# Kernel tuning notes

Measured on AMD Instinct MI355X. Metric: run time of the kernel, lower is better.

The kernel has to match this reference:

```python
import jax, jax.numpy as jnp
import numpy as np

DIM = 512
DIM_INPUTS = (8,)*4 + (16,)*4 + (32,)*4 + (64,)*4 + (128,)*4 + (256,)*4  # 24 bands, sum=2016
N_BANDS = len(DIM_INPUTS)
TOTAL_OUT2 = 2 * sum(DIM_INPUTS)  # 4032 (concatenated last-layer gated width)
B, T = 4, 512


def _glu_tanh(z):
    # LinearGLUWithTanH epilogue: chunk last dim, tanh(a) * sigmoid(gate)
    a, gate = jnp.split(z, 2, axis=-1)
    return jnp.tanh(a) * jax.nn.sigmoid(gate)


def setup_inputs() -> dict:
    key = jax.random.key(0)
    k0, k1, k2, k3, k4 = jax.random.split(key, 5)
    x = jax.random.normal(k0, (B, T, N_BANDS, DIM), dtype=jnp.float32)
    # layer 0: per-band Linear(DIM, 2*DIM), stacked over bands
    W0 = jax.random.normal(k1, (N_BANDS, DIM, 2 * DIM), dtype=jnp.float32) / np.float32(np.sqrt(DIM))
    b0 = jax.random.normal(k2, (N_BANDS, 2 * DIM), dtype=jnp.float32) * 0.01
    # layer 1 (last): per-band Linear(DIM, 2*dim_in); widths differ, so pack
    # all bands' weight columns into one concatenated matrix sliced statically.
    W1 = jax.random.normal(k3, (DIM, TOTAL_OUT2), dtype=jnp.float32) / np.float32(np.sqrt(DIM))
    b1 = jax.random.normal(k4, (TOTAL_OUT2,), dtype=jnp.float32) * 0.01
    return {"x": x, "W0": W0, "b0": b0, "W1": W1, "b1": b1}


def reference(x, W0, b0, W1, b1):
    # layer 0 for all bands in one grouped GEMM: (b t n d),(n d e)->(b t n e)
    h = _glu_tanh(jnp.einsum('btnd,nde->btne', x, W0) + b0)  # (B,T,N,DIM)
    outs = []
    off = 0
    for i, di in enumerate(DIM_INPUTS):  # static loop over structurally distinct bands
        w = W1[:, off:off + 2 * di]
        bb = b1[off:off + 2 * di]
        outs.append(_glu_tanh(h[:, :, i] @ w + bb))  # (B,T,di)
        off += 2 * di
    return jnp.concatenate(outs, axis=-1)  # (B,T,sum(DIM_INPUTS))
```

## Files before the change

kernel.cpp:

```cpp
#include <hip/hip_runtime.h>
#include <cstdint>
#include <cstddef>


typedef _Float16 f16;
typedef _Float16 f16x8 __attribute__((ext_vector_type(8)));
typedef float floatx4 __attribute__((ext_vector_type(4)));

#define BT 2048
#define NB 24

__device__ __forceinline__ int band_di(int b){ return 8 << (b >> 2); }
__device__ __forceinline__ int band_off2(int b){
  int g = b >> 2;
  return 2 * (32 * ((1 << g) - 1) + (b & 3) * (8 << g));
}

__device__ __forceinline__ float fsigm(float x){
  return __builtin_amdgcn_rcpf(1.f + __expf(-x));
}
__device__ __forceinline__ float ftanh(float x){
  return 1.f - 2.f * __builtin_amdgcn_rcpf(1.f + __expf(2.f * x));
}

__device__ __forceinline__ void gl_lds16(const void* g, void* l){
  __builtin_amdgcn_global_load_lds(
      (const __attribute__((address_space(1))) unsigned int*)g,
      (__attribute__((address_space(3))) unsigned int*)l, 16, 0, 0);
}


__global__ __launch_bounds__(256) void cast_x(const float4* __restrict__ in,
                                              f16* __restrict__ out){
  int t = blockIdx.x * 256 + threadIdx.x;
  float4 v = in[t];
  typedef _Float16 f16x4 __attribute__((ext_vector_type(4)));
  f16x4 o = { (f16)v.x, (f16)v.y, (f16)v.z, (f16)v.w };
  *(f16x4*)(out + (size_t)t * 4) = o;
}

__global__ __launch_bounds__(256) void cast_w0(const float* __restrict__ W0,
                                               f16* __restrict__ w0t){
  __shared__ float tile[64][33];
  int bid = blockIdx.x;
  int dt   = bid & 7;
  int half = (bid >> 3) & 1;
  int g    = (bid >> 4) & 15;
  int band = bid >> 8;
  int t = threadIdx.x;
  int c0 = half * 512 + g * 32;
  int d0 = dt * 64;
  int r  = t >> 2;
  int cs = (t & 3) * 8;
  const float* src = W0 + ((size_t)(band * 512 + d0 + r)) * 1024 + c0 + cs;
  float4 v0 = *(const float4*)src;
  float4 v1 = *(const float4*)(src + 4);
  tile[r][cs + 0] = v0.x; tile[r][cs + 1] = v0.y; tile[r][cs + 2] = v0.z; tile[r][cs + 3] = v0.w;
  tile[r][cs + 4] = v1.x; tile[r][cs + 5] = v1.y; tile[r][cs + 6] = v1.z; tile[r][cs + 7] = v1.w;
  __syncthreads();
  int i   = t >> 3;
  int ds8 = (t & 7) * 8;
  int prow = g * 64 + 2 * i + half;
  f16x8 o;
  #pragma unroll
  for (int k = 0; k < 8; ++k) o[k] = (f16)tile[ds8 + k][i];
  *(f16x8*)(w0t + ((size_t)(band * 1024 + prow)) * 512 + d0 + ds8) = o;
}

__global__ __launch_bounds__(256) void cast_w1(const float* __restrict__ W1,
                                               f16* __restrict__ w1t){
  __shared__ f16 tile[16][520];
  int jt = blockIdx.x;
  int j16 = jt * 16;
  int band = 23;
  for (int b = 0; b < 24; ++b){ if (j16 < band_off2(b + 1)) { band = b; break; } }
  int off2 = band_off2(band), di = band_di(band);
  int p0 = j16 - off2;
  int oca = off2 + (p0 >> 1);
  int ocg = oca + di;
  int t = threadIdx.x;
  #pragma unroll
  for (int hh = 0; hh < 2; ++hh){
    int d = hh * 256 + t;
    const float* rowp = W1 + (size_t)d * 4032;
    float4 a0 = *(const float4*)(rowp + oca);
    float4 a1 = *(const float4*)(rowp + oca + 4);
    float4 g0 = *(const float4*)(rowp + ocg);
    float4 g1 = *(const float4*)(rowp + ocg + 4);
    float av[8] = {a0.x,a0.y,a0.z,a0.w,a1.x,a1.y,a1.z,a1.w};
    float gv[8] = {g0.x,g0.y,g0.z,g0.w,g1.x,g1.y,g1.z,g1.w};
    #pragma unroll
    for (int q = 0; q < 8; ++q){
      tile[2*q][d]   = (f16)av[q];
      tile[2*q+1][d] = (f16)gv[q];
    }
  }
  __syncthreads();
  int j = t & 15, dc = (t >> 4) * 32;
  f16x8 o[4];
  #pragma unroll
  for (int k = 0; k < 4; ++k) o[k] = *(const f16x8*)&tile[j][dc + k*8];
  f16* dst = w1t + (size_t)(j16 + j) * 512 + dc;
  #pragma unroll
  for (int k = 0; k < 4; ++k) *(f16x8*)(dst + k*8) = o[k];
}

__global__ __launch_bounds__(256) void cast_bias(const float* __restrict__ b0,
                                                 const float* __restrict__ b1,
                                                 float* __restrict__ b0p,
                                                 float* __restrict__ b1p){
  int t = blockIdx.x * 256 + threadIdx.x;
  if (t < NB * 1024){
    int p = t & 1023;
    int base = t & ~1023;
    b0p[t] = b0[base + ((p & 1) ? 512 + (p >> 1) : (p >> 1))];
  } else {
    int j = t - NB * 1024;
    if (j < 4032){
      int band = 23;
      for (int b = 0; b < 24; ++b){ if (j < band_off2(b + 1)) { band = b; break; } }
      int off2 = band_off2(band);
      int di = band_di(band);
      int p = j - off2;
      b1p[j] = b1[off2 + ((p & 1) ? di + (p >> 1) : (p >> 1))];
    }
  }
}

__global__ __launch_bounds__(256) void gemm1(const f16* __restrict__ xh,
                                             const f16* __restrict__ w0t,
                                             const float* __restrict__ b0p,
                                             f16* __restrict__ h){
  __shared__ __align__(16) f16 As[128 * 64];
  __shared__ __align__(16) f16 Bs[128 * 64];
  int bid = blockIdx.x;
  int wid = (bid & 7) * 384 + (bid >> 3);
  int band = wid >> 7;
  int mt = (wid >> 3) & 15;
  int nt = wid & 7;
  int t = threadIdx.x;
  int lane = t & 63, w = t >> 6;
  int wm = w & 1, wn = w >> 1;
  int quad = lane >> 4, lc = lane & 15;
  const int mrow0 = mt * 128;
  const int nrow0 = nt * 128;

  const char* gA[4]; const char* gB[4];
  f16* lA[4]; f16* lB[4];
  #pragma unroll
  for (int p = 0; p < 4; ++p){
    int idx = p * 256 + t;
    int r = idx >> 3, s = idx & 7, l = s ^ (r & 7);
    gA[p] = (const char*)(xh + ((size_t)(mrow0 + r) * 24 + band) * 512 + l * 8);
    gB[p] = (const char*)(w0t + ((size_t)(band * 1024 + nrow0 + r)) * 512 + l * 8);
    lA[p] = &As[idx * 8];
    lB[p] = &Bs[idx * 8];
  }
  int aoff[4], boff[4];
  #pragma unroll
  for (int i = 0; i < 4; ++i){
    int m = wm * 64 + i * 16 + lc;
    aoff[i] = (m * 64 + ((quad ^ (m & 7)) << 3)) * 2;
    int n = wn * 64 + i * 16 + lc;
    boff[i] = (n * 64 + ((quad ^ (n & 7)) << 3)) * 2;
  }
  const char* Ab = (const char*)As;
  const char* Bb = (const char*)Bs;

  floatx4 acc[4][4];
  #pragma unroll
  for (int i = 0; i < 4; ++i)
    #pragma unroll
    for (int j = 0; j < 4; ++j) acc[i][j] = floatx4{0.f, 0.f, 0.f, 0.f};

  for (int kb = 0; kb < 8; ++kb){
    #pragma unroll
    for (int p = 0; p < 4; ++p){ gl_lds16(gA[p], lA[p]); gA[p] += 128; }
    #pragma unroll
    for (int p = 0; p < 4; ++p){ gl_lds16(gB[p], lB[p]); gB[p] += 128; }
    __syncthreads();
    #pragma unroll
    for (int s2 = 0; s2 < 2; ++s2){
      f16x8 af[4], bf[4];
      #pragma unroll
      for (int i = 0; i < 4; ++i){
        af[i] = *(const f16x8*)(Ab + (aoff[i] ^ (s2 * 64)));
        bf[i] = *(const f16x8*)(Bb + (boff[i] ^ (s2 * 64)));
      }
      #pragma unroll
      for (int i = 0; i < 4; ++i)
        #pragma unroll
        for (int j = 0; j < 4; ++j)
          acc[i][j] = __builtin_amdgcn_mfma_f32_16x16x32_f16(af[i], bf[j], acc[i][j], 0, 0, 0);
    }
    __syncthreads();
  }
  #pragma unroll
  for (int j = 0; j < 4; ++j){
    int colp = nrow0 + wn * 64 + j * 16 + lc;
    float bias = b0p[band * 1024 + colp];
    #pragma unroll
    for (int i = 0; i < 4; ++i){
      int mbase = mrow0 + wm * 64 + i * 16 + quad * 4;
      #pragma unroll
      for (int r = 0; r < 4; ++r){
        float z = acc[i][j][r] + bias;
        float zp = __shfl_xor(z, 1);
        if (!(lc & 1)){
          float hv = ftanh(z) * fsigm(zp);
          h[((size_t)band * BT + mbase + r) * 512 + (colp >> 1)] = (f16)hv;
        }
      }
    }
  }
}

template<int BN>
__device__ __forceinline__ void gemm2_tile(const f16* __restrict__ hb,
                                           const f16* __restrict__ w1t,
                                           const float* __restrict__ b1p,
                                           float* __restrict__ out,
                                           int band, int mt, int ntile,
                                           f16* As, f16* Bs){
  constexpr int WNW = (BN == 128) ? 2 : 1;
  constexpr int WMW = 4 / WNW;
  constexpr int MF = 128 / (WMW * 16);
  constexpr int NF = BN / (WNW * 16);
  int t = threadIdx.x;
  int lane = t & 63, w = t >> 6;
  int wm = (WNW == 2) ? (w & 1) : w;
  int wn = (WNW == 2) ? (w >> 1) : 0;
  int quad = lane >> 4, lc = lane & 15;
  int off2 = band_off2(band);
  int jbase = off2 + ntile * BN;

  constexpr int BCH = BN * 8;
  constexpr int BP = (BCH + 255) / 256;
  const char* gA[4]; const char* gB[BP];
  f16* lA[4]; f16* lB[BP];
  #pragma unroll
  for (int p = 0; p < 4; ++p){
    int idx = p * 256 + t;
    int r = idx >> 3, s = idx & 7, l = s ^ (r & 7);
    gA[p] = (const char*)(hb + ((size_t)(mt * 128 + r)) * 512 + l * 8);
    lA[p] = &As[idx * 8];
  }
  #pragma unroll
  for (int p = 0; p < BP; ++p){
    int idx = p * 256 + t;
    int r = idx >> 3, s = idx & 7, l = s ^ (r & 7);
    gB[p] = (const char*)(w1t + ((size_t)(jbase + r)) * 512 + l * 8);
    lB[p] = &Bs[idx * 8];
  }
  int aoff[MF], boff[NF];
  #pragma unroll
  for (int i = 0; i < MF; ++i){
    int m = wm * (MF * 16) + i * 16 + lc;
    aoff[i] = (m * 64 + ((quad ^ (m & 7)) << 3)) * 2;
  }
  #pragma unroll
  for (int j = 0; j < NF; ++j){
    int n = wn * (NF * 16) + j * 16 + lc;
    boff[j] = (n * 64 + ((quad ^ (n & 7)) << 3)) * 2;
  }
  const char* Ab = (const char*)As;
  const char* Bb = (const char*)Bs;

  floatx4 acc[MF][NF];
  #pragma unroll
  for (int i = 0; i < MF; ++i)
    #pragma unroll
    for (int j = 0; j < NF; ++j) acc[i][j] = floatx4{0.f, 0.f, 0.f, 0.f};

  for (int kb = 0; kb < 8; ++kb){
    #pragma unroll
    for (int p = 0; p < 4; ++p){ gl_lds16(gA[p], lA[p]); gA[p] += 128; }
    #pragma unroll
    for (int p = 0; p < BP; ++p){
      if ((BCH % 256 == 0) || (p * 256 + t) < BCH){
        gl_lds16(gB[p], lB[p]); gB[p] += 128;
      }
    }
    __syncthreads();
    #pragma unroll
    for (int s2 = 0; s2 < 2; ++s2){
      f16x8 af[MF], bf[NF];
      #pragma unroll
      for (int i = 0; i < MF; ++i)
        af[i] = *(const f16x8*)(Ab + (aoff[i] ^ (s2 * 64)));
      #pragma unroll
      for (int j = 0; j < NF; ++j)
        bf[j] = *(const f16x8*)(Bb + (boff[j] ^ (s2 * 64)));
      #pragma unroll
      for (int i = 0; i < MF; ++i)
        #pragma unroll
        for (int j = 0; j < NF; ++j)
          acc[i][j] = __builtin_amdgcn_mfma_f32_16x16x32_f16(af[i], bf[j], acc[i][j], 0, 0, 0);
    }
    __syncthreads();
  }
  int outbase = off2 >> 1;
  #pragma unroll
  for (int j = 0; j < NF; ++j){
    int p = ntile * BN + wn * (NF * 16) + j * 16 + lc;
    float bias = b1p[off2 + p];
    #pragma unroll
    for (int i = 0; i < MF; ++i){
      int mbase = mt * 128 + wm * (MF * 16) + i * 16 + quad * 4;
      #pragma unroll
      for (int r = 0; r < 4; ++r){
        float z = acc[i][j][r] + bias;
        float zp = __shfl_xor(z, 1);
        if (!(lc & 1)){
          out[(size_t)(mbase + r) * 2016 + outbase + (p >> 1)] = ftanh(z) * fsigm(zp);
        }
      }
    }
  }
}

__global__ __launch_bounds__(256) void gemm2(const f16* __restrict__ h,
                                             const f16* __restrict__ w1t,
                                             const float* __restrict__ b1p,
                                             float* __restrict__ out){
  __shared__ __align__(16) f16 As[128 * 64];
  __shared__ __align__(16) f16 Bs[128 * 64];
  int bid = blockIdx.x;
  int band, mt, ntile, cls;
  if (bid < 256){
    band = bid >> 4; mt = bid & 15; ntile = 0; cls = band >> 2;
  } else if (bid < 384){
    int rel = bid - 256; band = 16 + (rel >> 5);
    int r2 = rel & 31; mt = r2 & 15; ntile = r2 >> 4; cls = 4;
  } else {
    int rel = bid - 384; band = 20 + (rel >> 6);
    int r2 = rel & 63; mt = r2 & 15; ntile = r2 >> 4; cls = 5;
  }
  const f16* hb = h + ((size_t)band << 20);
  switch (cls){
    case 0:  gemm2_tile<16 >(hb, w1t, b1p, out, band, mt, ntile, As, Bs); break;
    case 1:  gemm2_tile<32 >(hb, w1t, b1p, out, band, mt, ntile, As, Bs); break;
    case 2:  gemm2_tile<64 >(hb, w1t, b1p, out, band, mt, ntile, As, Bs); break;
    default: gemm2_tile<128>(hb, w1t, b1p, out, band, mt, ntile, As, Bs); break;
  }
}

extern "C" void kernel_launch(void* const* d_in, const int* in_sizes, int n_in,
                              void* d_out, int out_size, void* d_ws, size_t ws_size,
                              hipStream_t stream){
  const float* x  = (const float*)d_in[0];
  const float* W0 = (const float*)d_in[1];
  const float* b0 = (const float*)d_in[2];
  const float* W1 = (const float*)d_in[3];
  const float* b1 = (const float*)d_in[4];
  char* ws = (char*)d_ws;
  f16*   xh   = (f16*)(ws);
  f16*   hbuf = (f16*)(ws + 50331648);
  f16*   w0t  = (f16*)(ws + 100663296);
  f16*   w1t  = (f16*)(ws + 125829120);
  float* b0p  = (float*)(ws + 129957888);
  float* b1p  = (float*)(ws + 130056192);

  cast_x   <<<24576, 256, 0, stream>>>((const float4*)x, xh);
  cast_w0  <<<6144,  256, 0, stream>>>(W0, w0t);
  cast_w1  <<<252,   256, 0, stream>>>(W1, w1t);
  cast_bias<<<112,   256, 0, stream>>>(b0, b1, b0p, b1p);
  gemm1    <<<3072,  256, 0, stream>>>(xh, w0t, b0p, hbuf);
  gemm2    <<<640,   256, 0, stream>>>(hbuf, w1t, b1p, (float*)d_out);
}
```

Baseline: 317.6 us.

## Fuse prep casts into one kernel and load GEMM fragments directly from global

Merges the four cast kernels into a single prep launch and reorders x to a band-major f16 layout during the cast. Both GEMMs drop the LDS staging through global_load_lds and instead have each lane read its MFMA fragments straight from global memory, relying on cache hits and removing the barriers. The GLU epilogue now evaluates tanh or sigmoid once per lane before the shuffle, so no lane computes both. Without LDS, operand reuse across waves depends on L1/L2 hits, and the per-lane 16-byte strided reads may be less efficient than the staged tiles.

```diff
diff --git a/kernel.cpp b/kernel.cpp
--- a/kernel.cpp
+++ b/kernel.cpp
@@ -23,116 +23,117 @@
   return 1.f - 2.f * __builtin_amdgcn_rcpf(1.f + __expf(2.f * x));
 }
 
-__device__ __forceinline__ void gl_lds16(const void* g, void* l){
-  __builtin_amdgcn_global_load_lds(
-      (const __attribute__((address_space(1))) unsigned int*)g,
-      (__attribute__((address_space(3))) unsigned int*)l, 16, 0, 0);
-}
-
-
-__global__ __launch_bounds__(256) void cast_x(const float4* __restrict__ in,
-                                              f16* __restrict__ out){
-  int t = blockIdx.x * 256 + threadIdx.x;
-  float4 v = in[t];
-  typedef _Float16 f16x4 __attribute__((ext_vector_type(4)));
-  f16x4 o = { (f16)v.x, (f16)v.y, (f16)v.z, (f16)v.w };
-  *(f16x4*)(out + (size_t)t * 4) = o;
-}
-
-__global__ __launch_bounds__(256) void cast_w0(const float* __restrict__ W0,
-                                               f16* __restrict__ w0t){
-  __shared__ float tile[64][33];
+__global__ __launch_bounds__(256) void prep(const float* __restrict__ x,
+                                            const float* __restrict__ W0,
+                                            const float* __restrict__ W1,
+                                            const float* __restrict__ b0,
+                                            const float* __restrict__ b1,
+                                            f16* __restrict__ xh2,
+                                            f16* __restrict__ w0t,
+                                            f16* __restrict__ w1t,
+                                            float* __restrict__ b0p,
+                                            float* __restrict__ b1p){
+  __shared__ __align__(16) char smem[33792];
   int bid = blockIdx.x;
-  int dt   = bid & 7;
-  int half = (bid >> 3) & 1;
-  int g    = (bid >> 4) & 15;
-  int band = bid >> 8;
   int t = threadIdx.x;
-  int c0 = half * 512 + g * 32;
-  int d0 = dt * 64;
-  int r  = t >> 2;
-  int cs = (t & 3) * 8;
-  const float* src = W0 + ((size_t)(band * 512 + d0 + r)) * 1024 + c0 + cs;
-  float4 v0 = *(const float4*)src;
-  float4 v1 = *(const float4*)(src + 4);
-  tile[r][cs + 0] = v0.x; tile[r][cs + 1] = v0.y; tile[r][cs + 2] = v0.z; tile[r][cs + 3] = v0.w;
-  tile[r][cs + 4] = v1.x; tile[r][cs + 5] = v1.y; tile[r][cs + 6] = v1.z; tile[r][cs + 7] = v1.w;
-  __syncthreads();
-  int i   = t >> 3;
-  int ds8 = (t & 7) * 8;
-  int prow = g * 64 + 2 * i + half;
-  f16x8 o;
-  #pragma unroll
-  for (int k = 0; k < 8; ++k) o[k] = (f16)tile[ds8 + k][i];
-  *(f16x8*)(w0t + ((size_t)(band * 1024 + prow)) * 512 + d0 + ds8) = o;
-}
-
-__global__ __launch_bounds__(256) void cast_w1(const float* __restrict__ W1,
-                                               f16* __restrict__ w1t){
-  __shared__ f16 tile[16][520];
-  int jt = blockIdx.x;
-  int j16 = jt * 16;
-  int band = 23;
-  for (int b = 0; b < 24; ++b){ if (j16 < band_off2(b + 1)) { band = b; break; } }
-  int off2 = band_off2(band), di = band_di(band);
-  int p0 = j16 - off2;
-  int oca = off2 + (p0 >> 1);
-  int ocg = oca + di;
-  int t = threadIdx.x;
-  #pragma unroll
-  for (int hh = 0; hh < 2; ++hh){
-    int d = hh * 256 + t;
-    const float* rowp = W1 + (size_t)d * 4032;
-    float4 a0 = *(const float4*)(rowp + oca);
-    float4 a1 = *(const float4*)(rowp + oca + 4);
-    float4 g0 = *(const float4*)(rowp + ocg);
-    float4 g1 = *(const float4*)(rowp + ocg + 4);
-    float av[8] = {a0.x,a0.y,a0.z,a0.w,a1.x,a1.y,a1.z,a1.w};
-    float gv[8] = {g0.x,g0.y,g0.z,g0.w,g1.x,g1.y,g1.z,g1.w};
-    #pragma unroll
-    for (int q = 0; q < 8; ++q){
-      tile[2*q][d]   = (f16)av[q];
-      tile[2*q+1][d] = (f16)gv[q];
-    }
-  }
-  __syncthreads();
-  int j = t & 15, dc = (t >> 4) * 32;
-  f16x8 o[4];
-  #pragma unroll
-  for (int k = 0; k < 4; ++k) o[k] = *(const f16x8*)&tile[j][dc + k*8];
-  f16* dst = w1t + (size_t)(j16 + j) * 512 + dc;
-  #pragma unroll
-  for (int k = 0; k < 4; ++k) *(f16x8*)(dst + k*8) = o[k];
-}
-
-__global__ __launch_bounds__(256) void cast_bias(const float* __restrict__ b0,
-                                                 const float* __restrict__ b1,
-                                                 float* __restrict__ b0p,
-                                                 float* __restrict__ b1p){
-  int t = blockIdx.x * 256 + threadIdx.x;
-  if (t < NB * 1024){
-    int p = t & 1023;
-    int base = t & ~1023;
-    b0p[t] = b0[base + ((p & 1) ? 512 + (p >> 1) : (p >> 1))];
+  if (bid < 6144){
+    int r = bid / 3, bg = bid - 3 * r;
+    int band = bg * 8 + (t >> 5);
+    int k16 = (t & 31) * 16;
+    const float* src = x + ((size_t)(r * 24 + band)) * 512 + k16;
+    float4 v0 = *(const float4*)(src + 0);
+    float4 v1 = *(const float4*)(src + 4);
+    float4 v2 = *(const float4*)(src + 8);
+    float4 v3 = *(const float4*)(src + 12);
+    f16x8 o0 = { (f16)v0.x,(f16)v0.y,(f16)v0.z,(f16)v0.w,
+                 (f16)v1.x,(f16)v1.y,(f16)v1.z,(f16)v1.w };
+    f16x8 o1 = { (f16)v2.x,(f16)v2.y,(f16)v2.z,(f16)v2.w,
+                 (f16)v3.x,(f16)v3.y,(f16)v3.z,(f16)v3.w };
+    f16* dst = xh2 + ((size_t)(band * 2048 + r)) * 512 + k16;
+    *(f16x8*)(dst + 0) = o0;
+    *(f16x8*)(dst + 8) = o1;
+  } else if (bid < 12288){
+    float (*tile)[33] = (float(*)[33])smem;
+    int b2 = bid - 6144;
+    int dt   = b2 & 7;
+    int half = (b2 >> 3) & 1;
+    int g    = (b2 >> 4) & 15;
+    int band = b2 >> 8;
+    int c0 = half * 512 + g * 32;
+    int d0 = dt * 64;
+    int r  = t >> 2;
+    int cs = (t & 3) * 8;
+    const float* src = W0 + ((size_t)(band * 512 + d0 + r)) * 1024 + c0 + cs;
+    float4 v0 = *(const float4*)src;
+    float4 v1 = *(const float4*)(src + 4);
+    tile[r][cs+0]=v0.x; tile[r][cs+1]=v0.y; tile[r][cs+2]=v0.z; tile[r][cs+3]=v0.w;
+    tile[r][cs+4]=v1.x; tile[r][cs+5]=v1.y; tile[r][cs+6]=v1.z; tile[r][cs+7]=v1.w;
+    __syncthreads();
+    int i   = t >> 3;
+    int ds8 = (t & 7) * 8;
+    int prow = g * 64 + 2 * i + half;
+    f16x8 o;
+    #pragma unroll
+    for (int k = 0; k < 8; ++k) o[k] = (f16)tile[ds8 + k][i];
+    *(f16x8*)(w0t + ((size_t)(band * 1024 + prow)) * 512 + d0 + ds8) = o;
+  } else if (bid < 12540){
+    f16 (*tw)[520] = (f16(*)[520])smem;
+    int jt = bid - 12288;
+    int j16 = jt * 16;
+    int band = 23;
+    for (int b = 0; b < 24; ++b){ if (j16 < band_off2(b + 1)) { band = b; break; } }
+    int off2 = band_off2(band), di = band_di(band);
+    int p0 = j16 - off2;
+    int oca = off2 + (p0 >> 1);
+    int ocg = oca + di;
+    #pragma unroll
+    for (int hh = 0; hh < 2; ++hh){
+      int d = hh * 256 + t;
+      const float* rowp = W1 + (size_t)d * 4032;
+      float4 a0 = *(const float4*)(rowp + oca);
+      float4 a1 = *(const float4*)(rowp + oca + 4);
+      float4 g0 = *(const float4*)(rowp + ocg);
+      float4 g1 = *(const float4*)(rowp + ocg + 4);
+      float av[8] = {a0.x,a0.y,a0.z,a0.w,a1.x,a1.y,a1.z,a1.w};
+      float gv[8] = {g0.x,g0.y,g0.z,g0.w,g1.x,g1.y,g1.z,g1.w};
+      #pragma unroll
+      for (int q = 0; q < 8; ++q){
+        tw[2*q][d]   = (f16)av[q];
+        tw[2*q+1][d] = (f16)gv[q];
+      }
+    }
+    __syncthreads();
+    int j = t & 15, dc = (t >> 4) * 32;
+    f16x8 o[4];
+    #pragma unroll
+    for (int k = 0; k < 4; ++k) o[k] = *(const f16x8*)&tw[j][dc + k*8];
+    f16* dst = w1t + (size_t)(j16 + j) * 512 + dc;
+    #pragma unroll
+    for (int k = 0; k < 4; ++k) *(f16x8*)(dst + k*8) = o[k];
   } else {
-    int j = t - NB * 1024;
-    if (j < 4032){
-      int band = 23;
-      for (int b = 0; b < 24; ++b){ if (j < band_off2(b + 1)) { band = b; break; } }
-      int off2 = band_off2(band);
-      int di = band_di(band);
-      int p = j - off2;
-      b1p[j] = b1[off2 + ((p & 1) ? di + (p >> 1) : (p >> 1))];
-    }
-  }
-}
-
-__global__ __launch_bounds__(256) void gemm1(const f16* __restrict__ xh,
+    int idx = (bid - 12540) * 256 + t;
+    if (idx < NB * 1024){
+      int p = idx & 1023;
+      int base = idx & ~1023;
+      b0p[idx] = b0[base + ((p & 1) ? 512 + (p >> 1) : (p >> 1))];
+    } else {
+      int j = idx - NB * 1024;
+      if (j < 4032){
+        int band = 23;
+        for (int b = 0; b < 24; ++b){ if (j < band_off2(b + 1)) { band = b; break; } }
+        int off2 = band_off2(band);
+        int di = band_di(band);
+        int p = j - off2;
+        b1p[j] = b1[off2 + ((p & 1) ? di + (p >> 1) : (p >> 1))];
+      }
+    }
+  }
+}
+
+__global__ __launch_bounds__(256) void gemm1(const f16* __restrict__ xh2,
                                              const f16* __restrict__ w0t,
                                              const float* __restrict__ b0p,
                                              f16* __restrict__ h){
-  __shared__ __align__(16) f16 As[128 * 64];
-  __shared__ __align__(16) f16 Bs[128 * 64];
   int bid = blockIdx.x;
   int wid = (bid & 7) * 384 + (bid >> 3);
   int band = wid >> 7;
@@ -145,56 +146,32 @@
   const int mrow0 = mt * 128;
   const int nrow0 = nt * 128;
 
-  const char* gA[4]; const char* gB[4];
-  f16* lA[4]; f16* lB[4];
-  #pragma unroll
-  for (int p = 0; p < 4; ++p){
-    int idx = p * 256 + t;
-    int r = idx >> 3, s = idx & 7, l = s ^ (r & 7);
-    gA[p] = (const char*)(xh + ((size_t)(mrow0 + r) * 24 + band) * 512 + l * 8);
-    gB[p] = (const char*)(w0t + ((size_t)(band * 1024 + nrow0 + r)) * 512 + l * 8);
-    lA[p] = &As[idx * 8];
-    lB[p] = &Bs[idx * 8];
-  }
-  int aoff[4], boff[4];
+  const f16* pA[4]; const f16* pB[4];
   #pragma unroll
   for (int i = 0; i < 4; ++i){
-    int m = wm * 64 + i * 16 + lc;
-    aoff[i] = (m * 64 + ((quad ^ (m & 7)) << 3)) * 2;
-    int n = wn * 64 + i * 16 + lc;
-    boff[i] = (n * 64 + ((quad ^ (n & 7)) << 3)) * 2;
-  }
-  const char* Ab = (const char*)As;
-  const char* Bb = (const char*)Bs;
-
+    pA[i] = xh2 + ((size_t)(band * 2048 + mrow0 + wm * 64 + i * 16 + lc)) * 512 + quad * 8;
+    pB[i] = w0t + ((size_t)(band * 1024 + nrow0 + wn * 64 + i * 16 + lc)) * 512 + quad * 8;
+  }
   floatx4 acc[4][4];
   #pragma unroll
   for (int i = 0; i < 4; ++i)
     #pragma unroll
     for (int j = 0; j < 4; ++j) acc[i][j] = floatx4{0.f, 0.f, 0.f, 0.f};
 
-  for (int kb = 0; kb < 8; ++kb){
-    #pragma unroll
-    for (int p = 0; p < 4; ++p){ gl_lds16(gA[p], lA[p]); gA[p] += 128; }
-    #pragma unroll
-    for (int p = 0; p < 4; ++p){ gl_lds16(gB[p], lB[p]); gB[p] += 128; }
-    __syncthreads();
-    #pragma unroll
-    for (int s2 = 0; s2 < 2; ++s2){
-      f16x8 af[4], bf[4];
-      #pragma unroll
-      for (int i = 0; i < 4; ++i){
-        af[i] = *(const f16x8*)(Ab + (aoff[i] ^ (s2 * 64)));
-        bf[i] = *(const f16x8*)(Bb + (boff[i] ^ (s2 * 64)));
-      }
-      #pragma unroll
-      for (int i = 0; i < 4; ++i)
-        #pragma unroll
-        for (int j = 0; j < 4; ++j)
-          acc[i][j] = __builtin_amdgcn_mfma_f32_16x16x32_f16(af[i], bf[j], acc[i][j], 0, 0, 0);
-    }
-    __syncthreads();
-  }
+  #pragma unroll
+  for (int s = 0; s < 16; ++s){
+    f16x8 af[4], bf[4];
+    #pragma unroll
+    for (int i = 0; i < 4; ++i) af[i] = *(const f16x8*)(pA[i] + s * 32);
+    #pragma unroll
+    for (int i = 0; i < 4; ++i) bf[i] = *(const f16x8*)(pB[i] + s * 32);
+    #pragma unroll
+    for (int i = 0; i < 4; ++i)
+      #pragma unroll
+      for (int j = 0; j < 4; ++j)
+        acc[i][j] = __builtin_amdgcn_mfma_f32_16x16x32_f16(af[i], bf[j], acc[i][j], 0, 0, 0);
+  }
+
   #pragma unroll
   for (int j = 0; j < 4; ++j){
     int colp = nrow0 + wn * 64 + j * 16 + lc;
@@ -205,114 +182,70 @@
       #pragma unroll
       for (int r = 0; r < 4; ++r){
         float z = acc[i][j][r] + bias;
-        float zp = __shfl_xor(z, 1);
+        float v = (lc & 1) ? fsigm(z) : ftanh(z);
+        float vp = __shfl_xor(v, 1);
         if (!(lc & 1)){
-          float hv = ftanh(z) * fsigm(zp);
-          h[((size_t)band * BT + mbase + r) * 512 + (colp >> 1)] = (f16)hv;
+          h[((size_t)band * BT + mbase + r) * 512 + (colp >> 1)] = (f16)(v * vp);
         }
       }
     }
   }
 }
 
-template<int BN>
-__device__ __forceinline__ void gemm2_tile(const f16* __restrict__ hb,
-                                           const f16* __restrict__ w1t,
-                                           const float* __restrict__ b1p,
-                                           float* __restrict__ out,
-                                           int band, int mt, int ntile,
-                                           f16* As, f16* Bs){
-  constexpr int WNW = (BN == 128) ? 2 : 1;
-  constexpr int WMW = 4 / WNW;
-  constexpr int MF = 128 / (WMW * 16);
-  constexpr int NF = BN / (WNW * 16);
+template<int NF2>
+__device__ __forceinline__ void gemm2_direct(const f16* __restrict__ hb,
+                                             const f16* __restrict__ w1t,
+                                             const float* __restrict__ b1p,
+                                             float* __restrict__ out,
+                                             int band, int mt, int joff){
   int t = threadIdx.x;
   int lane = t & 63, w = t >> 6;
-  int wm = (WNW == 2) ? (w & 1) : w;
-  int wn = (WNW == 2) ? (w >> 1) : 0;
   int quad = lane >> 4, lc = lane & 15;
   int off2 = band_off2(band);
-  int jbase = off2 + ntile * BN;
-
-  constexpr int BCH = BN * 8;
-  constexpr int BP = (BCH + 255) / 256;
-  const char* gA[4]; const char* gB[BP];
-  f16* lA[4]; f16* lB[BP];
-  #pragma unroll
-  for (int p = 0; p < 4; ++p){
-    int idx = p * 256 + t;
-    int r = idx >> 3, s = idx & 7, l = s ^ (r & 7);
-    gA[p] = (const char*)(hb + ((size_t)(mt * 128 + r)) * 512 + l * 8);
-    lA[p] = &As[idx * 8];
-  }
-  #pragma unroll
-  for (int p = 0; p < BP; ++p){
-    int idx = p * 256 + t;
-    int r = idx >> 3, s = idx & 7, l = s ^ (r & 7);
-    gB[p] = (const char*)(w1t + ((size_t)(jbase + r)) * 512 + l * 8);
-    lB[p] = &Bs[idx * 8];
-  }
-  int aoff[MF], boff[NF];
-  #pragma unroll
-  for (int i = 0; i < MF; ++i){
-    int m = wm * (MF * 16) + i * 16 + lc;
-    aoff[i] = (m * 64 + ((quad ^ (m & 7)) << 3)) * 2;
-  }
-  #pragma unroll
-  for (int j = 0; j < NF; ++j){
-    int n = wn * (NF * 16) + j * 16 + lc;
-    boff[j] = (n * 64 + ((quad ^ (n & 7)) << 3)) * 2;
-  }
-  const char* Ab = (const char*)As;
-  const char* Bb = (const char*)Bs;
-
-  floatx4 acc[MF][NF];
-  #pragma unroll
-  for (int i = 0; i < MF; ++i)
-    #pragma unroll
-    for (int j = 0; j < NF; ++j) acc[i][j] = floatx4{0.f, 0.f, 0.f, 0.f};
-
-  for (int kb = 0; kb < 8; ++kb){
-    #pragma unroll
-    for (int p = 0; p < 4; ++p){ gl_lds16(gA[p], lA[p]); gA[p] += 128; }
-    #pragma unroll
-    for (int p = 0; p < BP; ++p){
-      if ((BCH % 256 == 0) || (p * 256 + t) < BCH){
-        gl_lds16(gB[p], lB[p]); gB[p] += 128;
-      }
-    }
-    __syncthreads();
-    #pragma unroll
-    for (int s2 = 0; s2 < 2; ++s2){
-      f16x8 af[MF], bf[NF];
-      #pragma unroll
-      for (int i = 0; i < MF; ++i)
-        af[i] = *(const f16x8*)(Ab + (aoff[i] ^ (s2 * 64)));
-      #pragma unroll
-      for (int j = 0; j < NF; ++j)
-        bf[j] = *(const f16x8*)(Bb + (boff[j] ^ (s2 * 64)));
-      #pragma unroll
-      for (int i = 0; i < MF; ++i)
-        #pragma unroll
-        for (int j = 0; j < NF; ++j)
-          acc[i][j] = __builtin_amdgcn_mfma_f32_16x16x32_f16(af[i], bf[j], acc[i][j], 0, 0, 0);
-    }
-    __syncthreads();
+  int jbase = off2 + joff;
+
+  const f16* pA[2]; const f16* pB[NF2];
+  #pragma unroll
+  for (int i = 0; i < 2; ++i)
+    pA[i] = hb + ((size_t)(mt * 128 + w * 32 + i * 16 + lc)) * 512 + quad * 8;
+  #pragma unroll
+  for (int j = 0; j < NF2; ++j)
+    pB[j] = w1t + ((size_t)(jbase + j * 16 + lc)) * 512 + quad * 8;
+
+  floatx4 acc[2][NF2];
+  #pragma unroll
+  for (int i = 0; i < 2; ++i)
+    #pragma unroll
+    for (int j = 0; j < NF2; ++j) acc[i][j] = floatx4{0.f, 0.f, 0.f, 0.f};
+
+  #pragma unroll
+  for (int s = 0; s < 16; ++s){
+    f16x8 af[2], bf[NF2];
+    #pragma unroll
+    for (int i = 0; i < 2; ++i) af[i] = *(const f16x8*)(pA[i] + s * 32);
+    #pragma unroll
+    for (int j = 0; j < NF2; ++j) bf[j] = *(const f16x8*)(pB[j] + s * 32);
+    #pragma unroll
+    for (int i = 0; i < 2; ++i)
+      #pragma unroll
+      for (int j = 0; j < NF2; ++j)
+        acc[i][j] = __builtin_amdgcn_mfma_f32_16x16x32_f16(af[i], bf[j], acc[i][j], 0, 0, 0);
   }
   int outbase = off2 >> 1;
   #pragma unroll
-  for (int j = 0; j < NF; ++j){
-    int p = ntile * BN + wn * (NF * 16) + j * 16 + lc;
+  for (int j = 0; j < NF2; ++j){
+    int p = joff + j * 16 + lc;
     float bias = b1p[off2 + p];
     #pragma unroll
-    for (int i = 0; i < MF; ++i){
-      int mbase = mt * 128 + wm * (MF * 16) + i * 16 + quad * 4;
+    for (int i = 0; i < 2; ++i){
+      int mbase = mt * 128 + w * 32 + i * 16 + quad * 4;
       #pragma unroll
       for (int r = 0; r < 4; ++r){
         float z = acc[i][j][r] + bias;
-        float zp = __shfl_xor(z, 1);
+        float v = (lc & 1) ? fsigm(z) : ftanh(z);
+        float vp = __shfl_xor(v, 1);
         if (!(lc & 1)){
-          out[(size_t)(mbase + r) * 2016 + outbase + (p >> 1)] = ftanh(z) * fsigm(zp);
+          out[(size_t)(mbase + r) * 2016 + outbase + (p >> 1)] = v * vp;
         }
       }
     }
@@ -323,25 +256,23 @@
                                              const f16* __restrict__ w1t,
                                              const float* __restrict__ b1p,
                                              float* __restrict__ out){
-  __shared__ __align__(16) f16 As[128 * 64];
-  __shared__ __align__(16) f16 Bs[128 * 64];
   int bid = blockIdx.x;
-  int band, mt, ntile, cls;
+  int band, mt, joff, cls;
   if (bid < 256){
-    band = bid >> 4; mt = bid & 15; ntile = 0; cls = band >> 2;
+    band = bid >> 4; mt = bid & 15; joff = 0; cls = band >> 2;
   } else if (bid < 384){
     int rel = bid - 256; band = 16 + (rel >> 5);
-    int r2 = rel & 31; mt = r2 & 15; ntile = r2 >> 4; cls = 4;
+    int r2 = rel & 31; mt = r2 & 15; joff = (r2 >> 4) * 128; cls = 3;
   } else {
     int rel = bid - 384; band = 20 + (rel >> 6);
-    int r2 = rel & 63; mt = r2 & 15; ntile = r2 >> 4; cls = 5;
+    int r2 = rel & 63; mt = r2 & 15; joff = (r2 >> 4) * 128; cls = 3;
   }
   const f16* hb = h + ((size_t)band << 20);
   switch (cls){
-    case 0:  gemm2_tile<16 >(hb, w1t, b1p, out, band, mt, ntile, As, Bs); break;
-    case 1:  gemm2_tile<32 >(hb, w1t, b1p, out, band, mt, ntile, As, Bs); break;
-    case 2:  gemm2_tile<64 >(hb, w1t, b1p, out, band, mt, ntile, As, Bs); break;
-    default: gemm2_tile<128>(hb, w1t, b1p, out, band, mt, ntile, As, Bs); break;
+    case 0:  gemm2_direct<1>(hb, w1t, b1p, out, band, mt, joff); break;
+    case 1:  gemm2_direct<2>(hb, w1t, b1p, out, band, mt, joff); break;
+    case 2:  gemm2_direct<4>(hb, w1t, b1p, out, band, mt, joff); break;
+    default: gemm2_direct<8>(hb, w1t, b1p, out, band, mt, joff); break;
   }
 }
 
@@ -354,17 +285,14 @@
   const float* W1 = (const float*)d_in[3];
   const float* b1 = (const float*)d_in[4];
   char* ws = (char*)d_ws;
-  f16*   xh   = (f16*)(ws);
+  f16*   xh2  = (f16*)(ws);
   f16*   hbuf = (f16*)(ws + 50331648);
   f16*   w0t  = (f16*)(ws + 100663296);
   f16*   w1t  = (f16*)(ws + 125829120);
   float* b0p  = (float*)(ws + 129957888);
   float* b1p  = (float*)(ws + 130056192);
 
-  cast_x   <<<24576, 256, 0, stream>>>((const float4*)x, xh);
-  cast_w0  <<<6144,  256, 0, stream>>>(W0, w0t);
-  cast_w1  <<<252,   256, 0, stream>>>(W1, w1t);
-  cast_bias<<<112,   256, 0, stream>>>(b0, b1, b0p, b1p);
-  gemm1    <<<3072,  256, 0, stream>>>(xh, w0t, b0p, hbuf);
-  gemm2    <<<640,   256, 0, stream>>>(hbuf, w1t, b1p, (float*)d_out);
-}
+  prep <<<12652, 256, 0, stream>>>(x, W0, W1, b0, b1, xh2, w0t, w1t, b0p, b1p);
+  gemm1<<<3072,  256, 0, stream>>>(xh2, w0t, b0p, hbuf);
+  gemm2<<<640,   256, 0, stream>>>(hbuf, w1t, b1p, (float*)d_out);
+}
```

Result: slower. 441.3 us (+38.9%).
